# Kernel optimization log

Hardware: AMD Instinct MI355X
Metric: run time of the kernel (lower is better)

The kernel has to match this reference:

```python
import jax, jax.numpy as jnp
import numpy as np

NEG_SLOPE = 0.2  # PyG GATConv default negative_slope
EPS = 1e-16      # PyG softmax denominator epsilon


def gat_conv(x, src, dst, W, b, att_src, att_dst, num_nodes):
    """PyG GATConv, heads=1, add_self_loops=True (self loops already in src/dst).
    x: [N, Fin]; src/dst: [E]; W: [Fin, Fout]; att_src/att_dst: [Fout]."""
    h = x @ W                                  # [N, Fout]
    a_src = h @ att_src                        # [N]
    a_dst = h @ att_dst                        # [N]
    e = jax.nn.leaky_relu(a_src[src] + a_dst[dst], NEG_SLOPE)  # [E]
    m = jax.ops.segment_max(e, dst, num_segments=num_nodes)    # softmax over edges grouped by dst
    ex = jnp.exp(e - m[dst])
    denom = jax.ops.segment_sum(ex, dst, num_segments=num_nodes)
    alpha = ex / (denom[dst] + EPS)            # [E]
    out = jax.ops.segment_sum(alpha[:, None] * h[src], dst, num_segments=num_nodes)
    return out + b


def global_attention(x, gate_w, gate_b):
    """PyG GlobalAttention with a single graph: softmax(gate_nn(x)) weighted sum."""
    gate = x @ gate_w + gate_b                 # [N, 1]
    attn = jax.nn.softmax(gate, axis=0)        # softmax over all nodes (one graph)
    return jnp.sum(attn * x, axis=0, keepdims=True)  # [1, F]


def setup_inputs() -> dict:
    key = jax.random.key(0)
    ks = jax.random.split(key, 12)
    N, E, D, H = 50000, 800000, 768, 256
    x = jax.random.normal(ks[0], (N, D), dtype=jnp.float32)
    edge_index = jax.random.randint(ks[1], (2, E), 0, N, dtype=jnp.int64)
    s = 1.0 / np.sqrt(D)
    W1 = jax.random.normal(ks[2], (D, H), dtype=jnp.float32) * s
    b1 = jnp.zeros((H,), dtype=jnp.float32)
    as1 = jax.random.normal(ks[3], (H,), dtype=jnp.float32) * (1.0 / np.sqrt(H))
    ad1 = jax.random.normal(ks[4], (H,), dtype=jnp.float32) * (1.0 / np.sqrt(H))
    s2 = 1.0 / np.sqrt(H)
    W2 = jax.random.normal(ks[5], (H, H), dtype=jnp.float32) * s2
    b2 = jnp.zeros((H,), dtype=jnp.float32)
    as2 = jax.random.normal(ks[6], (H,), dtype=jnp.float32) * s2
    ad2 = jax.random.normal(ks[7], (H,), dtype=jnp.float32) * s2
    gate_w = jax.random.normal(ks[8], (H, 1), dtype=jnp.float32) * s2
    gate_b = jnp.zeros((1,), dtype=jnp.float32)
    return {"x": x, "edge_index": edge_index, "W1": W1, "b1": b1, "as1": as1,
            "ad1": ad1, "W2": W2, "b2": b2, "as2": as2, "ad2": ad2,
            "gate_w": gate_w, "gate_b": gate_b}


def reference(x, edge_index, W1, b1, as1, ad1, W2, b2, as2, ad2, gate_w, gate_b):
    N = x.shape[0]
    loops = jnp.arange(N, dtype=edge_index.dtype)
    src = jnp.concatenate([edge_index[0], loops])  # add self loops (GATConv default)
    dst = jnp.concatenate([edge_index[1], loops])
    h = gat_conv(x, src, dst, W1, b1, as1, ad1, N)
    h = jax.nn.relu(h)
    h = gat_conv(h, src, dst, W2, b2, as2, ad2, N)
    h = jax.nn.relu(h)
    return global_attention(h, gate_w, gate_b)   # [1, 256]
```

## Files before the change

### kernel.cpp

```cpp
#include <hip/hip_runtime.h>

#define WAVE 64
#define LRELU(x) ((x) > 0.0f ? (x) : 0.2f * (x))

typedef __attribute__((ext_vector_type(8))) short bf16x8;
typedef __attribute__((ext_vector_type(4))) float f32x4;

__device__ __forceinline__ void gld16(const void* g, void* l) {
    __builtin_amdgcn_global_load_lds((const __attribute__((address_space(1))) unsigned int*)g,
                                     (__attribute__((address_space(3))) unsigned int*)l,
                                     16, 0, 0);
}

__device__ __forceinline__ unsigned short f2bf_hi(float f) {
    unsigned u = __builtin_bit_cast(unsigned, f);
    u += 0x7FFF + ((u >> 16) & 1);
    return (unsigned short)(u >> 16);
}

__device__ __forceinline__ float4 bf4_to_f32(ushort4 v) {
    float4 r;
    r.x = __builtin_bit_cast(float, (unsigned)v.x << 16);
    r.y = __builtin_bit_cast(float, (unsigned)v.y << 16);
    r.z = __builtin_bit_cast(float, (unsigned)v.z << 16);
    r.w = __builtin_bit_cast(float, (unsigned)v.w << 16);
    return r;
}

__device__ __forceinline__ void split8(f32x4 a, f32x4 b, bf16x8& hi, bf16x8& lo) {
    float f[8] = {a[0], a[1], a[2], a[3], b[0], b[1], b[2], b[3]};
#pragma unroll
    for (int e = 0; e < 8; e++) {
        unsigned u = __builtin_bit_cast(unsigned, f[e]);
        unsigned t = u + 0x7FFF + ((u >> 16) & 1);
        float hf = __builtin_bit_cast(float, t & 0xFFFF0000u);
        float fl = f[e] - hf;
        unsigned u2 = __builtin_bit_cast(unsigned, fl);
        unsigned t2 = u2 + 0x7FFF + ((u2 >> 16) & 1);
        hi[e] = (short)(t >> 16);
        lo[e] = (short)(t2 >> 16);
    }
}

__global__ __launch_bounds__(256) void k_gemm_f32A(const float* __restrict__ A,
                                                   const unsigned short* __restrict__ Bh,
                                                   const unsigned short* __restrict__ Bl,
                                                   float* __restrict__ C,
                                                   unsigned short* __restrict__ Cb,
                                                   int M, int K) {
    __shared__ char smem[32768];
    char* SAH = smem;
    char* SAL = smem + 8192;
    char* SBH = smem + 16384;
    char* SBL = smem + 24576;

    const int tid = threadIdx.x, lane = tid & 63, w = tid >> 6;
    const int m16 = lane & 15, q = lane >> 4;
    const int row0 = blockIdx.x * 128, col0 = blockIdx.y * 128;

    f32x4 acc[4][4];
#pragma unroll
    for (int i = 0; i < 4; i++)
#pragma unroll
        for (int j = 0; j < 4; j++) acc[i][j] = (f32x4){0.f, 0.f, 0.f, 0.f};

    const int s_row = tid >> 1;
    const int s_mt  = s_row >> 4, s_m16 = s_row & 15;
    const int s_q0  = (tid & 1) * 2;
    int s_grow = row0 + s_row;
    if (s_grow > M - 1) s_grow = M - 1;
    const f32x4* aptr = (const f32x4*)&A[(size_t)s_grow * K] + (tid & 1) * 4;
    const int s_off = (s_mt * 4 + s_q0) * 256 + s_m16 * 16;

    const int b_rloc = lane >> 2;
    const int b_kb   = (lane & 3) * 16;

    f32x4 pre0 = aptr[0], pre1 = aptr[1], pre2 = aptr[2], pre3 = aptr[3];

    for (int k0 = 0; k0 < K; k0 += 32) {
#pragma unroll
        for (int s = 0; s < 2; s++) {
            int c = w * 2 + s;
            int brow = col0 + c * 16 + b_rloc;
            gld16((const char*)Bh + ((size_t)brow * K + k0) * 2 + b_kb, SBH + c * 1024);
            gld16((const char*)Bl + ((size_t)brow * K + k0) * 2 + b_kb, SBL + c * 1024);
        }
        {
            bf16x8 h0, l0, h1, l1;
            split8(pre0, pre1, h0, l0);
            split8(pre2, pre3, h1, l1);
            *(bf16x8*)(SAH + s_off)       = h0;
            *(bf16x8*)(SAL + s_off)       = l0;
            *(bf16x8*)(SAH + s_off + 256) = h1;
            *(bf16x8*)(SAL + s_off + 256) = l1;
        }
        __syncthreads();

        if (k0 + 32 < K) {
            aptr += 8;
            pre0 = aptr[0]; pre1 = aptr[1]; pre2 = aptr[2]; pre3 = aptr[3];
        }

        bf16x8 bh[4], bl[4];
#pragma unroll
        for (int nt = 0; nt < 4; nt++) {
            int r = (w & 1) * 64 + nt * 16 + m16;
            bh[nt] = *(bf16x8*)(SBH + r * 64 + q * 16);
            bl[nt] = *(bf16x8*)(SBL + r * 64 + q * 16);
        }
#pragma unroll
        for (int mt = 0; mt < 4; mt++) {
            int frag = ((w >> 1) * 4 + mt) * 4 + q;
            bf16x8 ah = *(bf16x8*)(SAH + frag * 256 + m16 * 16);
            bf16x8 al = *(bf16x8*)(SAL + frag * 256 + m16 * 16);
#pragma unroll
            for (int nt = 0; nt < 4; nt++) {
                acc[mt][nt] = __builtin_amdgcn_mfma_f32_16x16x32_bf16(ah, bh[nt], acc[mt][nt], 0, 0, 0);
                acc[mt][nt] = __builtin_amdgcn_mfma_f32_16x16x32_bf16(ah, bl[nt], acc[mt][nt], 0, 0, 0);
                acc[mt][nt] = __builtin_amdgcn_mfma_f32_16x16x32_bf16(al, bh[nt], acc[mt][nt], 0, 0, 0);
            }
        }
        __syncthreads();
    }

    const int rbase = row0 + (w >> 1) * 64;
    const int cbase = col0 + (w & 1) * 64;
#pragma unroll
    for (int mt = 0; mt < 4; mt++)
#pragma unroll
        for (int r = 0; r < 4; r++) {
            int row = rbase + mt * 16 + q * 4 + r;
            if (row < M) {
#pragma unroll
                for (int nt = 0; nt < 4; nt++) {
                    float v = acc[mt][nt][r];
                    C[(size_t)row * 256 + cbase + nt * 16 + m16] = v;
                    Cb[(size_t)row * 256 + cbase + nt * 16 + m16] = f2bf_hi(v);
                }
            }
        }
}

__global__ __launch_bounds__(256) void k_gemm_bf16A(const unsigned short* __restrict__ Ah,
                                                    const unsigned short* __restrict__ Al,
                                                    const unsigned short* __restrict__ Bh,
                                                    const unsigned short* __restrict__ Bl,
                                                    float* __restrict__ C,
                                                    unsigned short* __restrict__ Cb,
                                                    int M, int K) {
    __shared__ char smem[32768];
    char* SAH = smem;
    char* SAL = smem + 8192;
    char* SBH = smem + 16384;
    char* SBL = smem + 24576;

    const int tid = threadIdx.x, lane = tid & 63, w = tid >> 6;
    const int m16 = lane & 15, q = lane >> 4;
    const int row0 = blockIdx.x * 128, col0 = blockIdx.y * 128;

    f32x4 acc[4][4];
#pragma unroll
    for (int i = 0; i < 4; i++)
#pragma unroll
        for (int j = 0; j < 4; j++) acc[i][j] = (f32x4){0.f, 0.f, 0.f, 0.f};

    const int rloc = lane >> 2;
    const int kb   = (lane & 3) * 16;

    for (int k0 = 0; k0 < K; k0 += 32) {
#pragma unroll
        for (int s = 0; s < 2; s++) {
            int c = w * 2 + s;
            int arow = row0 + c * 16 + rloc;
            int brow = col0 + c * 16 + rloc;
            gld16((const char*)Ah + ((size_t)arow * K + k0) * 2 + kb, SAH + c * 1024);
            gld16((const char*)Al + ((size_t)arow * K + k0) * 2 + kb, SAL + c * 1024);
            gld16((const char*)Bh + ((size_t)brow * K + k0) * 2 + kb, SBH + c * 1024);
            gld16((const char*)Bl + ((size_t)brow * K + k0) * 2 + kb, SBL + c * 1024);
        }
        __syncthreads();

        bf16x8 bh[4], bl[4];
#pragma unroll
        for (int nt = 0; nt < 4; nt++) {
            int r = (w & 1) * 64 + nt * 16 + m16;
            bh[nt] = *(bf16x8*)(SBH + r * 64 + q * 16);
            bl[nt] = *(bf16x8*)(SBL + r * 64 + q * 16);
        }
#pragma unroll
        for (int mt = 0; mt < 4; mt++) {
            int r = (w >> 1) * 64 + mt * 16 + m16;
            bf16x8 ah = *(bf16x8*)(SAH + r * 64 + q * 16);
            bf16x8 al = *(bf16x8*)(SAL + r * 64 + q * 16);
#pragma unroll
            for (int nt = 0; nt < 4; nt++) {
                acc[mt][nt] = __builtin_amdgcn_mfma_f32_16x16x32_bf16(ah, bh[nt], acc[mt][nt], 0, 0, 0);
                acc[mt][nt] = __builtin_amdgcn_mfma_f32_16x16x32_bf16(ah, bl[nt], acc[mt][nt], 0, 0, 0);
                acc[mt][nt] = __builtin_amdgcn_mfma_f32_16x16x32_bf16(al, bh[nt], acc[mt][nt], 0, 0, 0);
            }
        }
        __syncthreads();
    }

    const int rbase = row0 + (w >> 1) * 64;
    const int cbase = col0 + (w & 1) * 64;
#pragma unroll
    for (int mt = 0; mt < 4; mt++)
#pragma unroll
        for (int r = 0; r < 4; r++) {
            int row = rbase + mt * 16 + q * 4 + r;
            if (row < M) {
#pragma unroll
                for (int nt = 0; nt < 4; nt++) {
                    float v = acc[mt][nt][r];
                    C[(size_t)row * 256 + cbase + nt * 16 + m16] = v;
                    Cb[(size_t)row * 256 + cbase + nt * 16 + m16] = f2bf_hi(v);
                }
            }
        }
}

__global__ __launch_bounds__(256) void k_convB(const float* __restrict__ W,
                                               unsigned short* __restrict__ BThi,
                                               unsigned short* __restrict__ BTlo, int K) {
    int idx = blockIdx.x * 256 + threadIdx.x;
    int k = idx >> 8, n = idx & 255;
    if (k >= K) return;
    float f = W[(size_t)k * 256 + n];
    unsigned u = __builtin_bit_cast(unsigned, f);
    unsigned t = u + 0x7FFF + ((u >> 16) & 1);
    float hf = __builtin_bit_cast(float, t & 0xFFFF0000u);
    unsigned short lb = f2bf_hi(f - hf);
    BThi[(size_t)n * K + k] = (unsigned short)(t >> 16);
    BTlo[(size_t)n * K + k] = lb;
}

__global__ __launch_bounds__(256) void k_att(const float* __restrict__ h,
                                             const float* __restrict__ att_s,
                                             const float* __restrict__ att_d,
                                             float* __restrict__ asrc,
                                             float* __restrict__ adst, int N) {
    int wid = threadIdx.x >> 6;
    int lane = threadIdx.x & 63;
    int node = blockIdx.x * 4 + wid;
    if (node >= N) return;
    float4 hv = *(const float4*)&h[(size_t)node * 256 + lane * 4];
    float4 sv = *(const float4*)&att_s[lane * 4];
    float4 dv = *(const float4*)&att_d[lane * 4];
    float s = hv.x * sv.x + hv.y * sv.y + hv.z * sv.z + hv.w * sv.w;
    float d = hv.x * dv.x + hv.y * dv.y + hv.z * dv.z + hv.w * dv.w;
#pragma unroll
    for (int off = 32; off; off >>= 1) {
        s += __shfl_xor(s, off);
        d += __shfl_xor(d, off);
    }
    if (lane == 0) { asrc[node] = s; adst[node] = d; }
}

__global__ __launch_bounds__(256) void k_degree(const int* __restrict__ dst,
                                                int* __restrict__ counts, int E) {
    int e = blockIdx.x * 256 + threadIdx.x;
    if (e < E) atomicAdd(&counts[dst[e]], 1);
}

__global__ __launch_bounds__(256) void k_part(const int* __restrict__ counts,
                                              int* __restrict__ psum, int N) {
    __shared__ int red[256];
    int tid = threadIdx.x;
    int i = blockIdx.x * 256 + tid;
    red[tid] = (i < N) ? counts[i] : 0;
    __syncthreads();
    for (int off = 128; off; off >>= 1) {
        if (tid < off) red[tid] += red[tid + off];
        __syncthreads();
    }
    if (tid == 0) psum[blockIdx.x] = red[0];
}

__global__ __launch_bounds__(256) void k_scan_part(int* __restrict__ psum, int nb,
                                                   int* __restrict__ total_out) {
    __shared__ int s[256];
    int tid = threadIdx.x;
    int v = (tid < nb) ? psum[tid] : 0;
    s[tid] = v;
    __syncthreads();
    for (int off = 1; off < 256; off <<= 1) {
        int t = (tid >= off) ? s[tid - off] : 0;
        __syncthreads();
        s[tid] += t;
        __syncthreads();
    }
    if (tid < nb) psum[tid] = s[tid] - v;
    if (tid == 255) *total_out = s[255];
}

__global__ __launch_bounds__(256) void k_rowptr(const int* __restrict__ counts,
                                                const int* __restrict__ psum,
                                                int* __restrict__ rowptr,
                                                int* __restrict__ cursor, int N) {
    __shared__ int s[256];
    int tid = threadIdx.x;
    int i = blockIdx.x * 256 + tid;
    int v = (i < N) ? counts[i] : 0;
    s[tid] = v;
    __syncthreads();
    for (int off = 1; off < 256; off <<= 1) {
        int t = (tid >= off) ? s[tid - off] : 0;
        __syncthreads();
        s[tid] += t;
        __syncthreads();
    }
    if (i < N) {
        int excl = psum[blockIdx.x] + s[tid] - v;
        rowptr[i] = excl;
        cursor[i] = excl;
    }
}

__global__ __launch_bounds__(256) void k_scatter(const int* __restrict__ src,
                                                 const int* __restrict__ dst,
                                                 int* __restrict__ cursor,
                                                 int* __restrict__ col, int E) {
    int e = blockIdx.x * 256 + threadIdx.x;
    if (e < E) {
        int p = atomicAdd(&cursor[dst[e]], 1);
        col[p] = src[e];
    }
}

__global__ __launch_bounds__(256) void k_alpha(const float* __restrict__ asrc,
                                               const float* __restrict__ adst,
                                               const int* __restrict__ rowptr,
                                               const int* __restrict__ col,
                                               float* __restrict__ walpha,
                                               float* __restrict__ wselfv,
                                               float* __restrict__ winvv, int N) {
    int wid = threadIdx.x >> 6;
    int lane = threadIdx.x & 63;
    int node = blockIdx.x * 4 + wid;
    if (node >= N) return;
    int start = rowptr[node], end = rowptr[node + 1];
    float ad = adst[node];
    float eself = asrc[node] + ad;
    eself = LRELU(eself);
    float m = eself;
    for (int j = start + lane; j < end; j += WAVE) {
        float e = asrc[col[j]] + ad;
        e = LRELU(e);
        m = fmaxf(m, e);
    }
#pragma unroll
    for (int off = 32; off; off >>= 1) m = fmaxf(m, __shfl_xor(m, off));
    float sum = 0.f;
    for (int j = start + lane; j < end; j += WAVE) {
        float e = asrc[col[j]] + ad;
        e = LRELU(e);
        float wgt = __expf(e - m);
        walpha[j] = wgt;
        sum += wgt;
    }
#pragma unroll
    for (int off = 32; off; off >>= 1) sum += __shfl_xor(sum, off);
    if (lane == 0) {
        float ws = __expf(eself - m);
        wselfv[node] = ws;
        winvv[node] = 1.0f / (sum + ws + 1e-16f);
    }
}

__global__ __launch_bounds__(256) void k_gather(const unsigned short* __restrict__ hb,
                                                const float* __restrict__ walpha,
                                                const float* __restrict__ wselfv,
                                                const float* __restrict__ winvv,
                                                const int* __restrict__ rowptr,
                                                const int* __restrict__ col,
                                                const float* __restrict__ bias,
                                                float* __restrict__ outf,
                                                unsigned short* __restrict__ outh,
                                                unsigned short* __restrict__ outl,
                                                const float* __restrict__ gw,
                                                const float* __restrict__ gb,
                                                float* __restrict__ gatep, int N) {
    int wid = threadIdx.x >> 6;
    int lane = threadIdx.x & 63;
    int node = blockIdx.x * 4 + wid;
    if (node >= N) return;
    int j = rowptr[node], end = rowptr[node + 1];
    float ws = wselfv[node];
    float4 hv = bf4_to_f32(*(const ushort4*)&hb[(size_t)node * 256 + lane * 4]);
    float ax = ws * hv.x, ay = ws * hv.y, az = ws * hv.z, aw = ws * hv.w;
    for (; j + 4 <= end; j += 4) {
        int s0 = col[j], s1 = col[j + 1], s2 = col[j + 2], s3 = col[j + 3];
        float w0 = walpha[j], w1 = walpha[j + 1], w2 = walpha[j + 2], w3 = walpha[j + 3];
        float4 h0 = bf4_to_f32(*(const ushort4*)&hb[(size_t)s0 * 256 + lane * 4]);
        float4 h1 = bf4_to_f32(*(const ushort4*)&hb[(size_t)s1 * 256 + lane * 4]);
        float4 h2 = bf4_to_f32(*(const ushort4*)&hb[(size_t)s2 * 256 + lane * 4]);
        float4 h3 = bf4_to_f32(*(const ushort4*)&hb[(size_t)s3 * 256 + lane * 4]);
        ax = fmaf(w0, h0.x, fmaf(w1, h1.x, fmaf(w2, h2.x, fmaf(w3, h3.x, ax))));
        ay = fmaf(w0, h0.y, fmaf(w1, h1.y, fmaf(w2, h2.y, fmaf(w3, h3.y, ay))));
        az = fmaf(w0, h0.z, fmaf(w1, h1.z, fmaf(w2, h2.z, fmaf(w3, h3.z, az))));
        aw = fmaf(w0, h0.w, fmaf(w1, h1.w, fmaf(w2, h2.w, fmaf(w3, h3.w, aw))));
    }
    for (; j < end; j++) {
        int s = col[j];
        float wgt = walpha[j];
        float4 hx = bf4_to_f32(*(const ushort4*)&hb[(size_t)s * 256 + lane * 4]);
        ax = fmaf(wgt, hx.x, ax); ay = fmaf(wgt, hx.y, ay);
        az = fmaf(wgt, hx.z, az); aw = fmaf(wgt, hx.w, aw);
    }
    float inv = winvv[node];
    float4 bv = *(const float4*)&bias[lane * 4];
    float ox = fmaxf(fmaf(ax, inv, bv.x), 0.0f);
    float oy = fmaxf(fmaf(ay, inv, bv.y), 0.0f);
    float oz = fmaxf(fmaf(az, inv, bv.z), 0.0f);
    float ow = fmaxf(fmaf(aw, inv, bv.w), 0.0f);
    if (outf) {
        float4 o = make_float4(ox, oy, oz, ow);
        *(float4*)&outf[(size_t)node * 256 + lane * 4] = o;
    }
    if (outh) {
        float of[4] = {ox, oy, oz, ow};
        unsigned long long ph = 0, pl = 0;
#pragma unroll
        for (int e = 0; e < 4; e++) {
            unsigned u = __builtin_bit_cast(unsigned, of[e]);
            unsigned t = u + 0x7FFF + ((u >> 16) & 1);
            float hf = __builtin_bit_cast(float, t & 0xFFFF0000u);
            float fl = of[e] - hf;
            unsigned u2 = __builtin_bit_cast(unsigned, fl);
            unsigned t2 = u2 + 0x7FFF + ((u2 >> 16) & 1);
            ph |= ((unsigned long long)(t >> 16)) << (16 * e);
            pl |= ((unsigned long long)(t2 >> 16)) << (16 * e);
        }
        *(unsigned long long*)&outh[(size_t)node * 256 + lane * 4] = ph;
        *(unsigned long long*)&outl[(size_t)node * 256 + lane * 4] = pl;
    }
    if (gatep) {
        float4 gv = *(const float4*)&gw[lane * 4];
        float s = ox * gv.x + oy * gv.y + oz * gv.z + ow * gv.w;
#pragma unroll
        for (int off = 32; off; off >>= 1) s += __shfl_xor(s, off);
        if (lane == 0) gatep[node] = s + gb[0];
    }
}

__global__ __launch_bounds__(256) void k_pmax(const float* __restrict__ gate, int N,
                                              float* __restrict__ pmax) {
    __shared__ float red[256];
    int tid = threadIdx.x;
    float m = -3.0e38f;
    for (int i = blockIdx.x * 256 + tid; i < N; i += gridDim.x * 256) m = fmaxf(m, gate[i]);
    red[tid] = m;
    __syncthreads();
    for (int off = 128; off; off >>= 1) {
        if (tid < off) red[tid] = fmaxf(red[tid], red[tid + off]);
        __syncthreads();
    }
    if (tid == 0) pmax[blockIdx.x] = red[0];
}

__global__ __launch_bounds__(256) void k_gmid(const float* __restrict__ pmax, int nb,
                                              float* __restrict__ scal,
                                              float* __restrict__ gout) {
    __shared__ float red[256];
    int tid = threadIdx.x;
    red[tid] = (tid < nb) ? pmax[tid] : -3.0e38f;
    __syncthreads();
    for (int off = 128; off; off >>= 1) {
        if (tid < off) red[tid] = fmaxf(red[tid], red[tid + off]);
        __syncthreads();
    }
    if (tid == 0) { scal[0] = red[0]; scal[1] = 0.0f; }
    gout[tid] = 0.0f;
}

__global__ __launch_bounds__(256) void k_gout(const float* __restrict__ h,
                                              const float* __restrict__ gate,
                                              float* __restrict__ scal_rw,
                                              float* __restrict__ gout, int N) {
    int f = threadIdx.x;
    float gmax = scal_rw[0];
    float acc = 0.0f, sumw = 0.0f;
    for (int i = blockIdx.x; i < N; i += gridDim.x) {
        float w = __expf(gate[i] - gmax);
        acc = fmaf(w, h[(size_t)i * 256 + f], acc);
        sumw += w;
    }
    atomicAdd(&gout[f], acc);
    if (f == 0) atomicAdd(&scal_rw[1], sumw);
}

__global__ __launch_bounds__(256) void k_final(const float* __restrict__ gout,
                                               const float* __restrict__ scal,
                                               float* __restrict__ out) {
    int f = threadIdx.x;
    out[f] = gout[f] / scal[1];
}

extern "C" void kernel_launch(void* const* d_in, const int* in_sizes, int n_in,
                              void* d_out, int out_size, void* d_ws, size_t ws_size,
                              hipStream_t stream) {
    const float* x   = (const float*)d_in[0];
    const int*   ei  = (const int*)d_in[1];
    const float* W1  = (const float*)d_in[2];
    const float* b1  = (const float*)d_in[3];
    const float* as1 = (const float*)d_in[4];
    const float* ad1 = (const float*)d_in[5];
    const float* W2  = (const float*)d_in[6];
    const float* b2  = (const float*)d_in[7];
    const float* as2 = (const float*)d_in[8];
    const float* ad2 = (const float*)d_in[9];
    const float* gw  = (const float*)d_in[10];
    const float* gb  = (const float*)d_in[11];
    float* out = (float*)d_out;

    const int N = in_sizes[0] / 768;
    const int E = in_sizes[1] / 2;
    const int Mpad = (N + 127) & ~127;
    const int* srcA = ei;
    const int* dstA = ei + E;

    char* w = (char*)d_ws;
    auto alloc = [&](size_t bytes) -> void* {
        void* p = (void*)w;
        w += (bytes + 255) & ~(size_t)255;
        return p;
    };
    float* bufH = (float*)alloc((size_t)N * 256 * 4);
    unsigned short* bufHb = (unsigned short*)alloc((size_t)N * 256 * 2);
    unsigned short* X2h = (unsigned short*)alloc((size_t)Mpad * 256 * 2);
    unsigned short* X2l = (unsigned short*)alloc((size_t)Mpad * 256 * 2);
    float* bufX = (float*)X2h;
    float* asrc   = (float*)alloc((size_t)N * 4);
    float* adst   = (float*)alloc((size_t)N * 4);
    float* gate   = (float*)alloc((size_t)N * 4);
    float* wselfv = (float*)alloc((size_t)N * 4);
    float* winvv  = (float*)alloc((size_t)N * 4);
    int*   counts = (int*)alloc((size_t)N * 4);
    int*   rowptr = (int*)alloc((size_t)(N + 1) * 4);
    int*   cursor = (int*)alloc((size_t)N * 4);
    int*   colbuf = (int*)alloc((size_t)E * 4);
    float* walpha = (float*)alloc((size_t)E * 4);
    int*   psum   = (int*)alloc(256 * 4);
    float* pmax   = (float*)alloc(256 * 4);
    float* scal   = (float*)alloc(8 * 4);
    float* gout   = (float*)alloc(256 * 4);
    unsigned short* BT1h = (unsigned short*)alloc((size_t)256 * 768 * 2);
    unsigned short* BT1l = (unsigned short*)alloc((size_t)256 * 768 * 2);
    unsigned short* BT2h = (unsigned short*)alloc((size_t)256 * 256 * 2);
    unsigned short* BT2l = (unsigned short*)alloc((size_t)256 * 256 * 2);

    const int eb  = (E + 255) / 256;
    const int nb4 = (N + 3) / 4;
    const int nb  = (N + 255) / 256;
    const dim3 gg(Mpad / 128, 2);

    k_convB<<<768, 256, 0, stream>>>(W1, BT1h, BT1l, 768);
    k_convB<<<256, 256, 0, stream>>>(W2, BT2h, BT2l, 256);

    (void)hipMemsetAsync(counts, 0, (size_t)N * 4, stream);
    k_degree<<<eb, 256, 0, stream>>>(dstA, counts, E);
    k_part<<<nb, 256, 0, stream>>>(counts, psum, N);
    k_scan_part<<<1, 256, 0, stream>>>(psum, nb, rowptr + N);
    k_rowptr<<<nb, 256, 0, stream>>>(counts, psum, rowptr, cursor, N);
    k_scatter<<<eb, 256, 0, stream>>>(srcA, dstA, cursor, colbuf, E);

    k_gemm_f32A<<<gg, 256, 0, stream>>>(x, BT1h, BT1l, bufH, bufHb, N, 768);
    k_att<<<nb4, 256, 0, stream>>>(bufH, as1, ad1, asrc, adst, N);
    k_alpha<<<nb4, 256, 0, stream>>>(asrc, adst, rowptr, colbuf, walpha, wselfv, winvv, N);
    k_gather<<<nb4, 256, 0, stream>>>(bufHb, walpha, wselfv, winvv, rowptr, colbuf, b1,
                                      nullptr, X2h, X2l, nullptr, nullptr, nullptr, N);

    k_gemm_bf16A<<<gg, 256, 0, stream>>>(X2h, X2l, BT2h, BT2l, bufH, bufHb, N, 256);
    k_att<<<nb4, 256, 0, stream>>>(bufH, as2, ad2, asrc, adst, N);
    k_alpha<<<nb4, 256, 0, stream>>>(asrc, adst, rowptr, colbuf, walpha, wselfv, winvv, N);
    k_gather<<<nb4, 256, 0, stream>>>(bufHb, walpha, wselfv, winvv, rowptr, colbuf, b2,
                                      bufX, nullptr, nullptr, gw, gb, gate, N);

    k_pmax<<<64, 256, 0, stream>>>(gate, N, pmax);
    k_gmid<<<1, 256, 0, stream>>>(pmax, 64, scal, gout);
    k_gout<<<256, 256, 0, stream>>>(bufX, gate, scal, gout, N);
    k_final<<<1, 256, 0, stream>>>(gout, scal, out);
}
```

Before: 671.5 us.

## Fuse attention dot products into GEMM epilogue and merge alpha with gather

The GEMM kernels no longer write an fp32 copy of h. Instead, their epilogue computes the per-row att_src/att_dst dot products with lane shuffles and adds them into asrc/adst with atomics, which are zeroed by memsets first. The separate alpha kernel is folded into the gather kernel, which recomputes exp weights on the fly and accumulates the denominator, so the walpha/wself/winv buffers go away. The hi part of the bf16 split now truncates instead of rounding, which saves ALU work but makes the lo residual carry more of the value. The changes remove kernel launches and the fp32 h write/read traffic, at the cost of atomics and some extra memsets.

```diff
diff --git a/kernel.cpp b/kernel.cpp
--- a/kernel.cpp
+++ b/kernel.cpp
@@ -32,12 +32,11 @@
 #pragma unroll
     for (int e = 0; e < 8; e++) {
         unsigned u = __builtin_bit_cast(unsigned, f[e]);
-        unsigned t = u + 0x7FFF + ((u >> 16) & 1);
-        float hf = __builtin_bit_cast(float, t & 0xFFFF0000u);
+        float hf = __builtin_bit_cast(float, u & 0xFFFF0000u);
         float fl = f[e] - hf;
         unsigned u2 = __builtin_bit_cast(unsigned, fl);
         unsigned t2 = u2 + 0x7FFF + ((u2 >> 16) & 1);
-        hi[e] = (short)(t >> 16);
+        hi[e] = (short)(u >> 16);
         lo[e] = (short)(t2 >> 16);
     }
 }
@@ -45,8 +44,11 @@
 __global__ __launch_bounds__(256) void k_gemm_f32A(const float* __restrict__ A,
                                                    const unsigned short* __restrict__ Bh,
                                                    const unsigned short* __restrict__ Bl,
-                                                   float* __restrict__ C,
                                                    unsigned short* __restrict__ Cb,
+                                                   float* __restrict__ asrc,
+                                                   float* __restrict__ adst,
+                                                   const float* __restrict__ att_s,
+                                                   const float* __restrict__ att_d,
                                                    int M, int K) {
     __shared__ char smem[32768];
     char* SAH = smem;
@@ -132,11 +134,36 @@
             int row = rbase + mt * 16 + q * 4 + r;
             if (row < M) {
 #pragma unroll
-                for (int nt = 0; nt < 4; nt++) {
-                    float v = acc[mt][nt][r];
-                    C[(size_t)row * 256 + cbase + nt * 16 + m16] = v;
-                    Cb[(size_t)row * 256 + cbase + nt * 16 + m16] = f2bf_hi(v);
-                }
+                for (int nt = 0; nt < 4; nt++)
+                    Cb[(size_t)row * 256 + cbase + nt * 16 + m16] = f2bf_hi(acc[mt][nt][r]);
+            }
+        }
+    float as_v[4], ad_v[4];
+#pragma unroll
+    for (int nt = 0; nt < 4; nt++) {
+        as_v[nt] = att_s[cbase + nt * 16 + m16];
+        ad_v[nt] = att_d[cbase + nt * 16 + m16];
+    }
+#pragma unroll
+    for (int mt = 0; mt < 4; mt++)
+#pragma unroll
+        for (int r = 0; r < 4; r++) {
+            float s = 0.f, d = 0.f;
+#pragma unroll
+            for (int nt = 0; nt < 4; nt++) {
+                float v = acc[mt][nt][r];
+                s = fmaf(v, as_v[nt], s);
+                d = fmaf(v, ad_v[nt], d);
+            }
+#pragma unroll
+            for (int off = 1; off < 16; off <<= 1) {
+                s += __shfl_xor(s, off);
+                d += __shfl_xor(d, off);
+            }
+            int row = rbase + mt * 16 + q * 4 + r;
+            if (m16 == 0 && row < M) {
+                atomicAdd(&asrc[row], s);
+                atomicAdd(&adst[row], d);
             }
         }
 }
@@ -145,8 +172,11 @@
                                                     const unsigned short* __restrict__ Al,
                                                     const unsigned short* __restrict__ Bh,
                                                     const unsigned short* __restrict__ Bl,
-                                                    float* __restrict__ C,
                                                     unsigned short* __restrict__ Cb,
+                                                    float* __restrict__ asrc,
+                                                    float* __restrict__ adst,
+                                                    const float* __restrict__ att_s,
+                                                    const float* __restrict__ att_d,
                                                     int M, int K) {
     __shared__ char smem[32768];
     char* SAH = smem;
@@ -211,11 +241,36 @@
             int row = rbase + mt * 16 + q * 4 + r;
             if (row < M) {
 #pragma unroll
-                for (int nt = 0; nt < 4; nt++) {
-                    float v = acc[mt][nt][r];
-                    C[(size_t)row * 256 + cbase + nt * 16 + m16] = v;
-                    Cb[(size_t)row * 256 + cbase + nt * 16 + m16] = f2bf_hi(v);
-                }
+                for (int nt = 0; nt < 4; nt++)
+                    Cb[(size_t)row * 256 + cbase + nt * 16 + m16] = f2bf_hi(acc[mt][nt][r]);
+            }
+        }
+    float as_v[4], ad_v[4];
+#pragma unroll
+    for (int nt = 0; nt < 4; nt++) {
+        as_v[nt] = att_s[cbase + nt * 16 + m16];
+        ad_v[nt] = att_d[cbase + nt * 16 + m16];
+    }
+#pragma unroll
+    for (int mt = 0; mt < 4; mt++)
+#pragma unroll
+        for (int r = 0; r < 4; r++) {
+            float s = 0.f, d = 0.f;
+#pragma unroll
+            for (int nt = 0; nt < 4; nt++) {
+                float v = acc[mt][nt][r];
+                s = fmaf(v, as_v[nt], s);
+                d = fmaf(v, ad_v[nt], d);
+            }
+#pragma unroll
+            for (int off = 1; off < 16; off <<= 1) {
+                s += __shfl_xor(s, off);
+                d += __shfl_xor(d, off);
+            }
+            int row = rbase + mt * 16 + q * 4 + r;
+            if (m16 == 0 && row < M) {
+                atomicAdd(&asrc[row], s);
+                atomicAdd(&adst[row], d);
             }
         }
 }
@@ -235,28 +290,6 @@
     BTlo[(size_t)n * K + k] = lb;
 }
 
-__global__ __launch_bounds__(256) void k_att(const float* __restrict__ h,
-                                             const float* __restrict__ att_s,
-                                             const float* __restrict__ att_d,
-                                             float* __restrict__ asrc,
-                                             float* __restrict__ adst, int N) {
-    int wid = threadIdx.x >> 6;
-    int lane = threadIdx.x & 63;
-    int node = blockIdx.x * 4 + wid;
-    if (node >= N) return;
-    float4 hv = *(const float4*)&h[(size_t)node * 256 + lane * 4];
-    float4 sv = *(const float4*)&att_s[lane * 4];
-    float4 dv = *(const float4*)&att_d[lane * 4];
-    float s = hv.x * sv.x + hv.y * sv.y + hv.z * sv.z + hv.w * sv.w;
-    float d = hv.x * dv.x + hv.y * dv.y + hv.z * dv.z + hv.w * dv.w;
-#pragma unroll
-    for (int off = 32; off; off >>= 1) {
-        s += __shfl_xor(s, off);
-        d += __shfl_xor(d, off);
-    }
-    if (lane == 0) { asrc[node] = s; adst[node] = d; }
-}
-
 __global__ __launch_bounds__(256) void k_degree(const int* __restrict__ dst,
                                                 int* __restrict__ counts, int E) {
     int e = blockIdx.x * 256 + threadIdx.x;
@@ -328,13 +361,18 @@
     }
 }
 
-__global__ __launch_bounds__(256) void k_alpha(const float* __restrict__ asrc,
-                                               const float* __restrict__ adst,
-                                               const int* __restrict__ rowptr,
-                                               const int* __restrict__ col,
-                                               float* __restrict__ walpha,
-                                               float* __restrict__ wselfv,
-                                               float* __restrict__ winvv, int N) {
+__global__ __launch_bounds__(256) void k_edge(const unsigned short* __restrict__ hb,
+                                              const float* __restrict__ asrc,
+                                              const float* __restrict__ adst,
+                                              const int* __restrict__ rowptr,
+                                              const int* __restrict__ col,
+                                              const float* __restrict__ bias,
+                                              float* __restrict__ outf,
+                                              unsigned short* __restrict__ outh,
+                                              unsigned short* __restrict__ outl,
+                                              const float* __restrict__ gw,
+                                              const float* __restrict__ gb,
+                                              float* __restrict__ gatep, int N) {
     int wid = threadIdx.x >> 6;
     int lane = threadIdx.x & 63;
     int node = blockIdx.x * 4 + wid;
@@ -351,47 +389,19 @@
     }
 #pragma unroll
     for (int off = 32; off; off >>= 1) m = fmaxf(m, __shfl_xor(m, off));
-    float sum = 0.f;
-    for (int j = start + lane; j < end; j += WAVE) {
-        float e = asrc[col[j]] + ad;
-        e = LRELU(e);
-        float wgt = __expf(e - m);
-        walpha[j] = wgt;
-        sum += wgt;
-    }
-#pragma unroll
-    for (int off = 32; off; off >>= 1) sum += __shfl_xor(sum, off);
-    if (lane == 0) {
-        float ws = __expf(eself - m);
-        wselfv[node] = ws;
-        winvv[node] = 1.0f / (sum + ws + 1e-16f);
-    }
-}
-
-__global__ __launch_bounds__(256) void k_gather(const unsigned short* __restrict__ hb,
-                                                const float* __restrict__ walpha,
-                                                const float* __restrict__ wselfv,
-                                                const float* __restrict__ winvv,
-                                                const int* __restrict__ rowptr,
-                                                const int* __restrict__ col,
-                                                const float* __restrict__ bias,
-                                                float* __restrict__ outf,
-                                                unsigned short* __restrict__ outh,
-                                                unsigned short* __restrict__ outl,
-                                                const float* __restrict__ gw,
-                                                const float* __restrict__ gb,
-                                                float* __restrict__ gatep, int N) {
-    int wid = threadIdx.x >> 6;
-    int lane = threadIdx.x & 63;
-    int node = blockIdx.x * 4 + wid;
-    if (node >= N) return;
-    int j = rowptr[node], end = rowptr[node + 1];
-    float ws = wselfv[node];
+
+    float wself = __expf(eself - m);
+    float denom = wself;
     float4 hv = bf4_to_f32(*(const ushort4*)&hb[(size_t)node * 256 + lane * 4]);
-    float ax = ws * hv.x, ay = ws * hv.y, az = ws * hv.z, aw = ws * hv.w;
+    float ax = wself * hv.x, ay = wself * hv.y, az = wself * hv.z, aw = wself * hv.w;
+    int j = start;
     for (; j + 4 <= end; j += 4) {
         int s0 = col[j], s1 = col[j + 1], s2 = col[j + 2], s3 = col[j + 3];
-        float w0 = walpha[j], w1 = walpha[j + 1], w2 = walpha[j + 2], w3 = walpha[j + 3];
+        float w0 = __expf(LRELU(asrc[s0] + ad) - m);
+        float w1 = __expf(LRELU(asrc[s1] + ad) - m);
+        float w2 = __expf(LRELU(asrc[s2] + ad) - m);
+        float w3 = __expf(LRELU(asrc[s3] + ad) - m);
+        denom += w0 + w1 + w2 + w3;
         float4 h0 = bf4_to_f32(*(const ushort4*)&hb[(size_t)s0 * 256 + lane * 4]);
         float4 h1 = bf4_to_f32(*(const ushort4*)&hb[(size_t)s1 * 256 + lane * 4]);
         float4 h2 = bf4_to_f32(*(const ushort4*)&hb[(size_t)s2 * 256 + lane * 4]);
@@ -403,12 +413,13 @@
     }
     for (; j < end; j++) {
         int s = col[j];
-        float wgt = walpha[j];
+        float wgt = __expf(LRELU(asrc[s] + ad) - m);
+        denom += wgt;
         float4 hx = bf4_to_f32(*(const ushort4*)&hb[(size_t)s * 256 + lane * 4]);
         ax = fmaf(wgt, hx.x, ax); ay = fmaf(wgt, hx.y, ay);
         az = fmaf(wgt, hx.z, az); aw = fmaf(wgt, hx.w, aw);
     }
-    float inv = winvv[node];
+    float inv = 1.0f / (denom + 1e-16f);
     float4 bv = *(const float4*)&bias[lane * 4];
     float ox = fmaxf(fmaf(ax, inv, bv.x), 0.0f);
     float oy = fmaxf(fmaf(ay, inv, bv.y), 0.0f);
@@ -526,7 +537,6 @@
         w += (bytes + 255) & ~(size_t)255;
         return p;
     };
-    float* bufH = (float*)alloc((size_t)N * 256 * 4);
     unsigned short* bufHb = (unsigned short*)alloc((size_t)N * 256 * 2);
     unsigned short* X2h = (unsigned short*)alloc((size_t)Mpad * 256 * 2);
     unsigned short* X2l = (unsigned short*)alloc((size_t)Mpad * 256 * 2);
@@ -534,13 +544,10 @@
     float* asrc   = (float*)alloc((size_t)N * 4);
     float* adst   = (float*)alloc((size_t)N * 4);
     float* gate   = (float*)alloc((size_t)N * 4);
-    float* wselfv = (float*)alloc((size_t)N * 4);
-    float* winvv  = (float*)alloc((size_t)N * 4);
     int*   counts = (int*)alloc((size_t)N * 4);
     int*   rowptr = (int*)alloc((size_t)(N + 1) * 4);
     int*   cursor = (int*)alloc((size_t)N * 4);
     int*   colbuf = (int*)alloc((size_t)E * 4);
-    float* walpha = (float*)alloc((size_t)E * 4);
     int*   psum   = (int*)alloc(256 * 4);
     float* pmax   = (float*)alloc(256 * 4);
     float* scal   = (float*)alloc(8 * 4);
@@ -565,17 +572,17 @@
     k_rowptr<<<nb, 256, 0, stream>>>(counts, psum, rowptr, cursor, N);
     k_scatter<<<eb, 256, 0, stream>>>(srcA, dstA, cursor, colbuf, E);
 
-    k_gemm_f32A<<<gg, 256, 0, stream>>>(x, BT1h, BT1l, bufH, bufHb, N, 768);
-    k_att<<<nb4, 256, 0, stream>>>(bufH, as1, ad1, asrc, adst, N);
-    k_alpha<<<nb4, 256, 0, stream>>>(asrc, adst, rowptr, colbuf, walpha, wselfv, winvv, N);
-    k_gather<<<nb4, 256, 0, stream>>>(bufHb, walpha, wselfv, winvv, rowptr, colbuf, b1,
-                                      nullptr, X2h, X2l, nullptr, nullptr, nullptr, N);
-
-    k_gemm_bf16A<<<gg, 256, 0, stream>>>(X2h, X2l, BT2h, BT2l, bufH, bufHb, N, 256);
-    k_att<<<nb4, 256, 0, stream>>>(bufH, as2, ad2, asrc, adst, N);
-    k_alpha<<<nb4, 256, 0, stream>>>(asrc, adst, rowptr, colbuf, walpha, wselfv, winvv, N);
-    k_gather<<<nb4, 256, 0, stream>>>(bufHb, walpha, wselfv, winvv, rowptr, colbuf, b2,
-                                      bufX, nullptr, nullptr, gw, gb, gate, N);
+    (void)hipMemsetAsync(asrc, 0, (size_t)N * 4, stream);
+    (void)hipMemsetAsync(adst, 0, (size_t)N * 4, stream);
+    k_gemm_f32A<<<gg, 256, 0, stream>>>(x, BT1h, BT1l, bufHb, asrc, adst, as1, ad1, N, 768);
+    k_edge<<<nb4, 256, 0, stream>>>(bufHb, asrc, adst, rowptr, colbuf, b1,
+                                    nullptr, X2h, X2l, nullptr, nullptr, nullptr, N);
+
+    (void)hipMemsetAsync(asrc, 0, (size_t)N * 4, stream);
+    (void)hipMemsetAsync(adst, 0, (size_t)N * 4, stream);
+    k_gemm_bf16A<<<gg, 256, 0, stream>>>(X2h, X2l, BT2h, BT2l, bufHb, asrc, adst, as2, ad2, N, 256);
+    k_edge<<<nb4, 256, 0, stream>>>(bufHb, asrc, adst, rowptr, colbuf, b2,
+                                    bufX, nullptr, nullptr, gw, gb, gate, N);
 
     k_pmax<<<64, 256, 0, stream>>>(gate, N, pmax);
     k_gmid<<<1, 256, 0, stream>>>(pmax, 64, scal, gout);
```

After: 629.9 us. 1.07x faster.
